# Kernel tuning notes

Measured on AMD Instinct MI355X. Metric: run time of the kernel, lower is better.

Reference implementation:

```python
import jax, jax.numpy as jnp
import numpy as np

N_NODES = 50000
F_IN = 96
HIDDEN = 128
OUT = 64
N_EDGES = 800000


def setup_inputs() -> dict:
    key = jax.random.key(0)
    ks = jax.random.split(key, 8)
    x = jax.random.normal(ks[0], (N_NODES, F_IN), dtype=jnp.float32)
    edge_index = jax.random.randint(ks[1], (2, N_EDGES), 0, N_NODES, dtype=jnp.int64)
    s = 1.0 / np.sqrt(F_IN)
    W1_rel = jax.random.uniform(ks[2], (HIDDEN, F_IN), minval=-s, maxval=s, dtype=jnp.float32)
    b1 = jax.random.uniform(ks[3], (HIDDEN,), minval=-s, maxval=s, dtype=jnp.float32)
    W1_root = jax.random.uniform(ks[4], (HIDDEN, F_IN), minval=-s, maxval=s, dtype=jnp.float32)
    s2 = 1.0 / np.sqrt(HIDDEN)
    W2_rel = jax.random.uniform(ks[5], (OUT, HIDDEN), minval=-s2, maxval=s2, dtype=jnp.float32)
    b2 = jax.random.uniform(ks[6], (OUT,), minval=-s2, maxval=s2, dtype=jnp.float32)
    W2_root = jax.random.uniform(ks[7], (OUT, HIDDEN), minval=-s2, maxval=s2, dtype=jnp.float32)
    return {"x": x, "edge_index": edge_index, "W1_rel": W1_rel, "b1": b1,
            "W1_root": W1_root, "W2_rel": W2_rel, "b2": b2, "W2_root": W2_root}


def _graph_conv(x, src, dst, mask, W_rel, b, W_root):
    # messages = x[src] (masked to remove self-loops), sum-aggregated at dst
    msgs = x[src] * mask  # [E, F]
    agg = jax.ops.segment_sum(msgs, dst, num_segments=x.shape[0])  # [N, F]
    return agg @ W_rel.T + b + x @ W_root.T


def reference(x, edge_index, W1_rel, b1, W1_root, W2_rel, b2, W2_root):
    src, dst = edge_index[0], edge_index[1]
    # remove_self_loops: zero out contributions of edges with src == dst
    mask = (src != dst).astype(x.dtype)[:, None]  # [E, 1]
    h = jax.nn.relu(_graph_conv(x, src, dst, mask, W1_rel, b1, W1_root))
    out = _graph_conv(h, src, dst, mask, W2_rel, b2, W2_root)
    return out
```

## Files before the change

kernel.cpp:

```cpp
#include <hip/hip_runtime.h>


#define N_NODES 50000
#define F_IN    96
#define HIDDEN  128
#define OUT_F   64

typedef __attribute__((ext_vector_type(8))) short short8;
typedef __attribute__((ext_vector_type(4))) float floatx4;

__device__ inline unsigned short f2bf(float f) {
    union { float f; unsigned u; } v; v.f = f;
    unsigned r = v.u + 0x7FFF + ((v.u >> 16) & 1);
    return (unsigned short)(r >> 16);
}
__device__ inline float bf2f(unsigned short b) {
    union { unsigned u; float f; } v; v.u = ((unsigned)b) << 16;
    return v.f;
}

__global__ __launch_bounds__(256) void setup_kernel(
    const float* __restrict__ x,
    const float* __restrict__ W1_rel, const float* __restrict__ W1_root,
    const float* __restrict__ W2_rel, const float* __restrict__ W2_root,
    unsigned short* __restrict__ xb, unsigned short* __restrict__ W1b,
    unsigned short* __restrict__ W2rb, unsigned short* __restrict__ W2sb,
    int* __restrict__ degz, int total8, int nzero)
{
    int i = blockIdx.x * 256 + threadIdx.x;
    if (i < total8) {
        const float4* p = (const float4*)(x + (size_t)i * 8);
        float4 v0 = p[0], v1 = p[1];
        short8 o;
        o[0] = (short)f2bf(v0.x); o[1] = (short)f2bf(v0.y);
        o[2] = (short)f2bf(v0.z); o[3] = (short)f2bf(v0.w);
        o[4] = (short)f2bf(v1.x); o[5] = (short)f2bf(v1.y);
        o[6] = (short)f2bf(v1.z); o[7] = (short)f2bf(v1.w);
        *(short8*)(xb + (size_t)i * 8) = o;
    }
    if (i < nzero) degz[i] = 0;
    if (i < 128 * 192) {
        int j = i / 192, k = i % 192;
        float v = (k < 96) ? W1_rel[j * 96 + k] : W1_root[j * 96 + k - 96];
        W1b[i] = f2bf(v);
    } else if (i < 128 * 192 + 64 * 128) {
        int i2 = i - 128 * 192;
        W2rb[i2] = f2bf(W2_rel[i2]);
    } else if (i < 128 * 192 + 2 * 64 * 128) {
        int i3 = i - 128 * 192 - 64 * 128;
        W2sb[i3] = f2bf(W2_root[i3]);
    }
}

__global__ __launch_bounds__(256) void deg_rank_kernel(
    const int* __restrict__ ei, int* __restrict__ deg,
    int* __restrict__ rank, int E)
{
    int i4 = blockIdx.x * 256 + threadIdx.x;
    int E4 = E >> 2;
    if (i4 < E4) {
        int4 s4 = ((const int4*)ei)[i4];
        int4 d4 = ((const int4*)(ei + E))[i4];
        int e0 = i4 * 4;
        int ss[4] = {s4.x, s4.y, s4.z, s4.w};
        int dd[4] = {d4.x, d4.y, d4.z, d4.w};
        #pragma unroll
        for (int k = 0; k < 4; ++k) {
            int s = ss[k], d = dd[k];
            if (s != d && (unsigned)d < (unsigned)N_NODES)
                rank[e0 + k] = atomicAdd(&deg[d], 1);
        }
    } else if (i4 == E4) {
        for (int e = E4 * 4; e < E; ++e) {
            int s = ei[e], d = ei[E + e];
            if (s != d && (unsigned)d < (unsigned)N_NODES)
                rank[e] = atomicAdd(&deg[d], 1);
        }
    }
}

__global__ __launch_bounds__(256) void alloc_kernel(
    const int* __restrict__ deg, int* __restrict__ off,
    int* __restrict__ counter, int N, int slice_size)
{
    int i = blockIdx.x * 256 + threadIdx.x;
    int lane = threadIdx.x & 63;
    int v = (i < N) ? deg[i] : 0;
    int s = v;
    #pragma unroll
    for (int d = 1; d < 64; d <<= 1) {
        int t = __shfl_up(s, d, 64);
        if (lane >= d) s += t;
    }
    int total = __shfl(s, 63, 64);
    int sl = (blockIdx.x * 256) / slice_size;
    int base = 0;
    if (lane == 63) base = atomicAdd(&counter[sl], total);
    base = __shfl(base, 63, 64);
    if (i < N) off[i] = base + s - v;
}

__global__ void scan8_kernel(const int* __restrict__ counter,
                             int* __restrict__ sbase)
{
    if (threadIdx.x == 0) {
        int run = 0;
        for (int s = 0; s < 8; ++s) { sbase[s] = run; run += counter[s]; }
    }
}

__global__ __launch_bounds__(256) void place_kernel(
    const int* __restrict__ ei, const int* __restrict__ off,
    const int* __restrict__ rank, const int* __restrict__ sbase,
    int* __restrict__ csr, int E, int slice_size)
{
    int sl = blockIdx.x & 7;
    int i4 = (blockIdx.x >> 3) * 256 + threadIdx.x;
    int sb = sbase[sl];
    int E4 = E >> 2;
    if (i4 < E4) {
        int4 d4 = ((const int4*)(ei + E))[i4];
        int e0 = i4 * 4;
        int dd[4] = {d4.x, d4.y, d4.z, d4.w};
        #pragma unroll
        for (int k = 0; k < 4; ++k) {
            int d = dd[k];
            if ((unsigned)d >= (unsigned)N_NODES) continue;
            if (d / slice_size != sl) continue;
            int e = e0 + k;
            int s = ei[e];
            if (s == d) continue;
            int p = sb + off[d] + rank[e];
            if ((unsigned)p < (unsigned)E)
                csr[p] = s;
        }
    } else if (i4 == E4) {
        for (int e = E4 * 4; e < E; ++e) {
            int d = ei[E + e];
            if ((unsigned)d >= (unsigned)N_NODES) continue;
            if (d / slice_size != sl) continue;
            int s = ei[e];
            if (s == d) continue;
            int p = sb + off[d] + rank[e];
            if ((unsigned)p < (unsigned)E)
                csr[p] = s;
        }
    }
}

template<int F>
__global__ __launch_bounds__(256) void gather_agg_bf(
    const unsigned short* __restrict__ feat, const int* __restrict__ off,
    const int* __restrict__ deg, const int* __restrict__ sbase,
    const int* __restrict__ csr, unsigned short* __restrict__ agg,
    int N, int E, int slice_size)
{
    constexpr int C = F / 8;
    int gid = blockIdx.x * 256 + threadIdx.x;
    int node = gid / C;
    int c = gid % C;
    if (node >= N) return;
    int j = sbase[node / slice_size] + off[node];
    int end = j + deg[node];
    if (j < 0) j = 0;
    if (end > E) end = E;
    float acc[8] = {};
    const unsigned short* fc = feat + c * 8;
    for (; j + 3 < end; j += 4) {
        int s0 = csr[j], s1 = csr[j + 1], s2 = csr[j + 2], s3 = csr[j + 3];
        short8 v0 = *(const short8*)(fc + (size_t)s0 * F);
        short8 v1 = *(const short8*)(fc + (size_t)s1 * F);
        short8 v2 = *(const short8*)(fc + (size_t)s2 * F);
        short8 v3 = *(const short8*)(fc + (size_t)s3 * F);
        #pragma unroll
        for (int i = 0; i < 8; ++i)
            acc[i] += (bf2f((unsigned short)v0[i]) + bf2f((unsigned short)v1[i]))
                    + (bf2f((unsigned short)v2[i]) + bf2f((unsigned short)v3[i]));
    }
    for (; j < end; ++j) {
        int s0 = csr[j];
        short8 v0 = *(const short8*)(fc + (size_t)s0 * F);
        #pragma unroll
        for (int i = 0; i < 8; ++i) acc[i] += bf2f((unsigned short)v0[i]);
    }
    short8 o;
    #pragma unroll
    for (int i = 0; i < 8; ++i) o[i] = (short)f2bf(acc[i]);
    *(short8*)(agg + (size_t)node * F + c * 8) = o;
}

template<int KT, int NO, bool SPLIT, bool RELU, bool HAS_BIAS, bool HAS_ADD, bool OUT_BF>
__global__ __launch_bounds__(256) void gemm_mfma(
    const unsigned short* __restrict__ A1, const unsigned short* __restrict__ A2,
    const unsigned short* __restrict__ W, const float* __restrict__ bias,
    const unsigned short* __restrict__ addb, void* __restrict__ out, int N)
{
    constexpr int NC = KT / 32;
    const int lane = threadIdx.x & 63;
    const int wave = threadIdx.x >> 6;
    const int node_base = blockIdx.x * 64 + wave * 16;
    const int m = lane & 15, quad = lane >> 4;
    int na = node_base + m;
    if (na >= N) na = N - 1;
    short8 a[NC];
    #pragma unroll
    for (int c = 0; c < NC; ++c) {
        if (SPLIT) {
            constexpr int HK = KT / 2;
            if (c < NC / 2)
                a[c] = *(const short8*)(A1 + (size_t)na * HK + c * 32 + quad * 8);
            else
                a[c] = *(const short8*)(A2 + (size_t)na * HK + (c - NC / 2) * 32 + quad * 8);
        } else {
            a[c] = *(const short8*)(A1 + (size_t)na * KT + c * 32 + quad * 8);
        }
    }
    #pragma unroll
    for (int jt = 0; jt < NO / 16; ++jt) {
        floatx4 acc = {0.f, 0.f, 0.f, 0.f};
        const unsigned short* wb = W + (size_t)(jt * 16 + m) * KT + quad * 8;
        #pragma unroll
        for (int c = 0; c < NC; ++c) {
            short8 b = *(const short8*)(wb + c * 32);
            acc = __builtin_amdgcn_mfma_f32_16x16x32_bf16(a[c], b, acc, 0, 0, 0);
        }
        int col = jt * 16 + m;
        float bv = HAS_BIAS ? bias[col] : 0.f;
        #pragma unroll
        for (int r = 0; r < 4; ++r) {
            int node = node_base + quad * 4 + r;
            if (node < N) {
                float v = acc[r] + bv;
                if (HAS_ADD) v += bf2f(addb[(size_t)node * NO + col]);
                if (RELU) v = fmaxf(v, 0.f);
                if (OUT_BF) ((unsigned short*)out)[(size_t)node * NO + col] = f2bf(v);
                else        ((float*)out)[(size_t)node * NO + col] = v;
            }
        }
    }
}

extern "C" void kernel_launch(void* const* d_in, const int* in_sizes, int n_in,
                              void* d_out, int out_size, void* d_ws, size_t ws_size,
                              hipStream_t stream) {
    const float* x       = (const float*)d_in[0];
    const int*   ei      = (const int*)d_in[1];
    const float* W1_rel  = (const float*)d_in[2];
    const float* b1      = (const float*)d_in[3];
    const float* W1_root = (const float*)d_in[4];
    const float* W2_rel  = (const float*)d_in[5];
    const float* b2      = (const float*)d_in[6];
    const float* W2_root = (const float*)d_in[7];
    float* out = (float*)d_out;

    const int N = in_sizes[0] / F_IN;
    const int E = in_sizes[1] / 2;
    const int slice_size = ((N + 2047) / 2048) * 256;

    char* ws = (char*)d_ws;
    size_t p = 0;
    unsigned short* xb    = (unsigned short*)(ws + p); p += (size_t)N_NODES * F_IN * 2;
    unsigned short* agg1b = (unsigned short*)(ws + p); p += (size_t)N_NODES * F_IN * 2;
    unsigned short* h     = (unsigned short*)(ws + p); p += (size_t)N_NODES * HIDDEN * 2;
    unsigned short* t     = (unsigned short*)(ws + p); p += (size_t)N_NODES * OUT_F * 2;
    unsigned short* agg2b = (unsigned short*)(ws + p); p += (size_t)N_NODES * OUT_F * 2;
    unsigned short* W1b   = (unsigned short*)(ws + p); p += (size_t)128 * 192 * 2;
    unsigned short* W2rb  = (unsigned short*)(ws + p); p += (size_t)64 * 128 * 2;
    unsigned short* W2sb  = (unsigned short*)(ws + p); p += (size_t)64 * 128 * 2;
    int* deg     = (int*)(ws + p);  p += (size_t)N_NODES * 4;
    int* counter = (int*)(ws + p);  p += 8 * 4;
    int* off     = (int*)(ws + p);  p += (size_t)N_NODES * 4;
    int* sbase   = (int*)(ws + p);  p += 8 * 4;
    int* rank    = (int*)(ws + p);  p += (size_t)800000 * 4;
    int* csr     = (int*)(ws + p);

    {
        int total8 = N * F_IN / 8;
        setup_kernel<<<(total8 + 255) / 256, 256, 0, stream>>>(
            x, W1_rel, W1_root, W2_rel, W2_root, xb, W1b, W2rb, W2sb,
            deg, total8, N + 8);
    }
    {
        int E4 = E >> 2;
        deg_rank_kernel<<<(E4 + 1 + 255) / 256, 256, 0, stream>>>(ei, deg, rank, E);
    }
    alloc_kernel<<<(N + 255) / 256, 256, 0, stream>>>(deg, off, counter, N, slice_size);
    scan8_kernel<<<1, 64, 0, stream>>>(counter, sbase);
    {
        int E4 = E >> 2;
        int bps = (E4 + 1 + 255) / 256;
        place_kernel<<<bps * 8, 256, 0, stream>>>(ei, off, rank, sbase, csr, E, slice_size);
    }

    const int gemm_blocks = (N + 63) / 64;

    {
        int total = N * (F_IN / 8);
        gather_agg_bf<F_IN><<<(total + 255) / 256, 256, 0, stream>>>(
            xb, off, deg, sbase, csr, agg1b, N, E, slice_size);
    }
    gemm_mfma<192, 128, true, true, true, false, true>
        <<<gemm_blocks, 256, 0, stream>>>(agg1b, xb, W1b, b1, nullptr, (void*)h, N);

    gemm_mfma<128, 64, false, false, false, false, true>
        <<<gemm_blocks, 256, 0, stream>>>(h, nullptr, W2rb, nullptr, nullptr, (void*)t, N);
    {
        int total = N * (OUT_F / 8);
        gather_agg_bf<OUT_F><<<(total + 255) / 256, 256, 0, stream>>>(
            t, off, deg, sbase, csr, agg2b, N, E, slice_size);
    }
    gemm_mfma<128, 64, false, false, true, true, false>
        <<<gemm_blocks, 256, 0, stream>>>(h, nullptr, W2sb, b2, agg2b, (void*)out, N);
}
```

Measured before the change: 246.2 us.

## Fuse all GNN stages into one cooperative persistent kernel with grid syncs

Replaces the nine separate kernel launches with a single cooperative persistent kernel whose phases are separated by grid.sync. It also fuses the first GEMM with the W2_rel GEMM through a shared-memory tile of h. It drops the scan8 pass by giving each slice a fixed CSR capacity region. The aim is to remove launch gaps and one full pass over h, at the cost of grid-wide barrier latency, a capped grid size, and a CSR layout that silently drops edges if one slice exceeds E/4.

Measured after the change: 687.9 us. 2.79x slower.

```diff
diff --git a/kernel.cpp b/kernel.cpp
--- a/kernel.cpp
+++ b/kernel.cpp
@@ -1,4 +1,7 @@
 #include <hip/hip_runtime.h>
+#include <hip/hip_cooperative_groups.h>
+
+namespace cg = cooperative_groups;
 
 
 #define N_NODES 50000
@@ -19,222 +22,290 @@
     return v.f;
 }
 
-__global__ __launch_bounds__(256) void setup_kernel(
-    const float* __restrict__ x,
-    const float* __restrict__ W1_rel, const float* __restrict__ W1_root,
-    const float* __restrict__ W2_rel, const float* __restrict__ W2_root,
-    unsigned short* __restrict__ xb, unsigned short* __restrict__ W1b,
-    unsigned short* __restrict__ W2rb, unsigned short* __restrict__ W2sb,
-    int* __restrict__ degz, int total8, int nzero)
-{
-    int i = blockIdx.x * 256 + threadIdx.x;
-    if (i < total8) {
-        const float4* p = (const float4*)(x + (size_t)i * 8);
-        float4 v0 = p[0], v1 = p[1];
-        short8 o;
-        o[0] = (short)f2bf(v0.x); o[1] = (short)f2bf(v0.y);
-        o[2] = (short)f2bf(v0.z); o[3] = (short)f2bf(v0.w);
-        o[4] = (short)f2bf(v1.x); o[5] = (short)f2bf(v1.y);
-        o[6] = (short)f2bf(v1.z); o[7] = (short)f2bf(v1.w);
-        *(short8*)(xb + (size_t)i * 8) = o;
-    }
-    if (i < nzero) degz[i] = 0;
-    if (i < 128 * 192) {
-        int j = i / 192, k = i % 192;
-        float v = (k < 96) ? W1_rel[j * 96 + k] : W1_root[j * 96 + k - 96];
-        W1b[i] = f2bf(v);
-    } else if (i < 128 * 192 + 64 * 128) {
-        int i2 = i - 128 * 192;
-        W2rb[i2] = f2bf(W2_rel[i2]);
-    } else if (i < 128 * 192 + 2 * 64 * 128) {
-        int i3 = i - 128 * 192 - 64 * 128;
-        W2sb[i3] = f2bf(W2_root[i3]);
-    }
-}
-
-__global__ __launch_bounds__(256) void deg_rank_kernel(
-    const int* __restrict__ ei, int* __restrict__ deg,
-    int* __restrict__ rank, int E)
-{
-    int i4 = blockIdx.x * 256 + threadIdx.x;
-    int E4 = E >> 2;
-    if (i4 < E4) {
-        int4 s4 = ((const int4*)ei)[i4];
-        int4 d4 = ((const int4*)(ei + E))[i4];
-        int e0 = i4 * 4;
-        int ss[4] = {s4.x, s4.y, s4.z, s4.w};
-        int dd[4] = {d4.x, d4.y, d4.z, d4.w};
-        #pragma unroll
-        for (int k = 0; k < 4; ++k) {
-            int s = ss[k], d = dd[k];
-            if (s != d && (unsigned)d < (unsigned)N_NODES)
-                rank[e0 + k] = atomicAdd(&deg[d], 1);
-        }
-    } else if (i4 == E4) {
-        for (int e = E4 * 4; e < E; ++e) {
-            int s = ei[e], d = ei[E + e];
-            if (s != d && (unsigned)d < (unsigned)N_NODES)
-                rank[e] = atomicAdd(&deg[d], 1);
-        }
-    }
-}
-
-__global__ __launch_bounds__(256) void alloc_kernel(
-    const int* __restrict__ deg, int* __restrict__ off,
-    int* __restrict__ counter, int N, int slice_size)
-{
-    int i = blockIdx.x * 256 + threadIdx.x;
-    int lane = threadIdx.x & 63;
-    int v = (i < N) ? deg[i] : 0;
-    int s = v;
-    #pragma unroll
-    for (int d = 1; d < 64; d <<= 1) {
-        int t = __shfl_up(s, d, 64);
-        if (lane >= d) s += t;
-    }
-    int total = __shfl(s, 63, 64);
-    int sl = (blockIdx.x * 256) / slice_size;
-    int base = 0;
-    if (lane == 63) base = atomicAdd(&counter[sl], total);
-    base = __shfl(base, 63, 64);
-    if (i < N) off[i] = base + s - v;
-}
-
-__global__ void scan8_kernel(const int* __restrict__ counter,
-                             int* __restrict__ sbase)
-{
-    if (threadIdx.x == 0) {
-        int run = 0;
-        for (int s = 0; s < 8; ++s) { sbase[s] = run; run += counter[s]; }
-    }
-}
-
-__global__ __launch_bounds__(256) void place_kernel(
-    const int* __restrict__ ei, const int* __restrict__ off,
-    const int* __restrict__ rank, const int* __restrict__ sbase,
-    int* __restrict__ csr, int E, int slice_size)
-{
-    int sl = blockIdx.x & 7;
-    int i4 = (blockIdx.x >> 3) * 256 + threadIdx.x;
-    int sb = sbase[sl];
-    int E4 = E >> 2;
-    if (i4 < E4) {
-        int4 d4 = ((const int4*)(ei + E))[i4];
-        int e0 = i4 * 4;
-        int dd[4] = {d4.x, d4.y, d4.z, d4.w};
-        #pragma unroll
-        for (int k = 0; k < 4; ++k) {
-            int d = dd[k];
-            if ((unsigned)d >= (unsigned)N_NODES) continue;
-            if (d / slice_size != sl) continue;
-            int e = e0 + k;
-            int s = ei[e];
-            if (s == d) continue;
-            int p = sb + off[d] + rank[e];
-            if ((unsigned)p < (unsigned)E)
-                csr[p] = s;
-        }
-    } else if (i4 == E4) {
-        for (int e = E4 * 4; e < E; ++e) {
-            int d = ei[E + e];
-            if ((unsigned)d >= (unsigned)N_NODES) continue;
-            if (d / slice_size != sl) continue;
-            int s = ei[e];
-            if (s == d) continue;
-            int p = sb + off[d] + rank[e];
-            if ((unsigned)p < (unsigned)E)
-                csr[p] = s;
-        }
-    }
-}
+struct MegaParams {
+    const float* x; const int* ei;
+    const float* W1_rel; const float* b1; const float* W1_root;
+    const float* W2_rel; const float* b2; const float* W2_root;
+    unsigned short* xb; unsigned short* agg1b; unsigned short* h;
+    unsigned short* t; unsigned short* agg2b;
+    unsigned short* W1b; unsigned short* W2rb; unsigned short* W2sb;
+    int* deg; int* counter; int* off; int* rank; int* csr;
+    float* out;
+    int N, E, slice_size, cap;
+};
 
 template<int F>
-__global__ __launch_bounds__(256) void gather_agg_bf(
-    const unsigned short* __restrict__ feat, const int* __restrict__ off,
-    const int* __restrict__ deg, const int* __restrict__ sbase,
-    const int* __restrict__ csr, unsigned short* __restrict__ agg,
-    int N, int E, int slice_size)
+__device__ void gather_phase(const unsigned short* __restrict__ feat,
+                             const int* __restrict__ off, const int* __restrict__ deg,
+                             const int* __restrict__ csr, unsigned short* __restrict__ agg,
+                             int N, int slice_size, int cap, int gtid, int gstride)
 {
     constexpr int C = F / 8;
-    int gid = blockIdx.x * 256 + threadIdx.x;
-    int node = gid / C;
-    int c = gid % C;
-    if (node >= N) return;
-    int j = sbase[node / slice_size] + off[node];
-    int end = j + deg[node];
-    if (j < 0) j = 0;
-    if (end > E) end = E;
-    float acc[8] = {};
-    const unsigned short* fc = feat + c * 8;
-    for (; j + 3 < end; j += 4) {
-        int s0 = csr[j], s1 = csr[j + 1], s2 = csr[j + 2], s3 = csr[j + 3];
-        short8 v0 = *(const short8*)(fc + (size_t)s0 * F);
-        short8 v1 = *(const short8*)(fc + (size_t)s1 * F);
-        short8 v2 = *(const short8*)(fc + (size_t)s2 * F);
-        short8 v3 = *(const short8*)(fc + (size_t)s3 * F);
+    const int total = N * C;
+    const int csr_total = 8 * cap;
+    for (int gid = gtid; gid < total; gid += gstride) {
+        int node = gid / C;
+        int c = gid % C;
+        int sl = node / slice_size;
+        int j = sl * cap + off[node];
+        int end = j + deg[node];
+        if (j < 0) j = 0;
+        if (end > csr_total) end = csr_total;
+        float acc[8] = {};
+        const unsigned short* fc = feat + c * 8;
+        for (; j + 3 < end; j += 4) {
+            int s0 = csr[j], s1 = csr[j + 1], s2 = csr[j + 2], s3 = csr[j + 3];
+            s0 = ((unsigned)s0 < (unsigned)N_NODES) ? s0 : 0;
+            s1 = ((unsigned)s1 < (unsigned)N_NODES) ? s1 : 0;
+            s2 = ((unsigned)s2 < (unsigned)N_NODES) ? s2 : 0;
+            s3 = ((unsigned)s3 < (unsigned)N_NODES) ? s3 : 0;
+            short8 v0 = *(const short8*)(fc + (size_t)s0 * F);
+            short8 v1 = *(const short8*)(fc + (size_t)s1 * F);
+            short8 v2 = *(const short8*)(fc + (size_t)s2 * F);
+            short8 v3 = *(const short8*)(fc + (size_t)s3 * F);
+            #pragma unroll
+            for (int i = 0; i < 8; ++i)
+                acc[i] += (bf2f((unsigned short)v0[i]) + bf2f((unsigned short)v1[i]))
+                        + (bf2f((unsigned short)v2[i]) + bf2f((unsigned short)v3[i]));
+        }
+        for (; j < end; ++j) {
+            int s0 = csr[j];
+            s0 = ((unsigned)s0 < (unsigned)N_NODES) ? s0 : 0;
+            short8 v0 = *(const short8*)(fc + (size_t)s0 * F);
+            #pragma unroll
+            for (int i = 0; i < 8; ++i) acc[i] += bf2f((unsigned short)v0[i]);
+        }
+        short8 o;
         #pragma unroll
-        for (int i = 0; i < 8; ++i)
-            acc[i] += (bf2f((unsigned short)v0[i]) + bf2f((unsigned short)v1[i]))
-                    + (bf2f((unsigned short)v2[i]) + bf2f((unsigned short)v3[i]));
-    }
-    for (; j < end; ++j) {
-        int s0 = csr[j];
-        short8 v0 = *(const short8*)(fc + (size_t)s0 * F);
-        #pragma unroll
-        for (int i = 0; i < 8; ++i) acc[i] += bf2f((unsigned short)v0[i]);
-    }
-    short8 o;
-    #pragma unroll
-    for (int i = 0; i < 8; ++i) o[i] = (short)f2bf(acc[i]);
-    *(short8*)(agg + (size_t)node * F + c * 8) = o;
-}
-
-template<int KT, int NO, bool SPLIT, bool RELU, bool HAS_BIAS, bool HAS_ADD, bool OUT_BF>
-__global__ __launch_bounds__(256) void gemm_mfma(
-    const unsigned short* __restrict__ A1, const unsigned short* __restrict__ A2,
-    const unsigned short* __restrict__ W, const float* __restrict__ bias,
-    const unsigned short* __restrict__ addb, void* __restrict__ out, int N)
+        for (int i = 0; i < 8; ++i) o[i] = (short)f2bf(acc[i]);
+        *(short8*)(agg + (size_t)node * F + c * 8) = o;
+    }
+}
+
+__global__ __launch_bounds__(256) void mega_kernel(MegaParams P)
 {
-    constexpr int NC = KT / 32;
-    const int lane = threadIdx.x & 63;
-    const int wave = threadIdx.x >> 6;
-    const int node_base = blockIdx.x * 64 + wave * 16;
+    cg::grid_group grid = cg::this_grid();
+    const int tid = threadIdx.x;
+    const int gtid = blockIdx.x * 256 + tid;
+    const int gstride = gridDim.x * 256;
+    const int lane = tid & 63;
+    const int wave = tid >> 6;
     const int m = lane & 15, quad = lane >> 4;
-    int na = node_base + m;
-    if (na >= N) na = N - 1;
-    short8 a[NC];
-    #pragma unroll
-    for (int c = 0; c < NC; ++c) {
-        if (SPLIT) {
-            constexpr int HK = KT / 2;
-            if (c < NC / 2)
-                a[c] = *(const short8*)(A1 + (size_t)na * HK + c * 32 + quad * 8);
-            else
-                a[c] = *(const short8*)(A2 + (size_t)na * HK + (c - NC / 2) * 32 + quad * 8);
-        } else {
-            a[c] = *(const short8*)(A1 + (size_t)na * KT + c * 32 + quad * 8);
-        }
-    }
-    #pragma unroll
-    for (int jt = 0; jt < NO / 16; ++jt) {
-        floatx4 acc = {0.f, 0.f, 0.f, 0.f};
-        const unsigned short* wb = W + (size_t)(jt * 16 + m) * KT + quad * 8;
-        #pragma unroll
-        for (int c = 0; c < NC; ++c) {
-            short8 b = *(const short8*)(wb + c * 32);
-            acc = __builtin_amdgcn_mfma_f32_16x16x32_bf16(a[c], b, acc, 0, 0, 0);
-        }
-        int col = jt * 16 + m;
-        float bv = HAS_BIAS ? bias[col] : 0.f;
-        #pragma unroll
-        for (int r = 0; r < 4; ++r) {
-            int node = node_base + quad * 4 + r;
-            if (node < N) {
-                float v = acc[r] + bv;
-                if (HAS_ADD) v += bf2f(addb[(size_t)node * NO + col]);
-                if (RELU) v = fmaxf(v, 0.f);
-                if (OUT_BF) ((unsigned short*)out)[(size_t)node * NO + col] = f2bf(v);
-                else        ((float*)out)[(size_t)node * NO + col] = v;
+    __shared__ __align__(16) unsigned short hs[4][16][136];
+
+    {
+        const int total8 = P.N * (F_IN / 8);
+        for (int i = gtid; i < total8; i += gstride) {
+            const float4* p = (const float4*)(P.x + (size_t)i * 8);
+            float4 v0 = p[0], v1 = p[1];
+            short8 o;
+            o[0] = (short)f2bf(v0.x); o[1] = (short)f2bf(v0.y);
+            o[2] = (short)f2bf(v0.z); o[3] = (short)f2bf(v0.w);
+            o[4] = (short)f2bf(v1.x); o[5] = (short)f2bf(v1.y);
+            o[6] = (short)f2bf(v1.z); o[7] = (short)f2bf(v1.w);
+            *(short8*)(P.xb + (size_t)i * 8) = o;
+        }
+        for (int i = gtid; i < P.N + 8; i += gstride) P.deg[i] = 0;
+        const int wtotal = 128 * 192 + 2 * 64 * 128;
+        for (int i = gtid; i < wtotal; i += gstride) {
+            if (i < 128 * 192) {
+                int j = i / 192, k = i % 192;
+                float v = (k < 96) ? P.W1_rel[j * 96 + k] : P.W1_root[j * 96 + k - 96];
+                P.W1b[i] = f2bf(v);
+            } else if (i < 128 * 192 + 64 * 128) {
+                int i2 = i - 128 * 192;
+                P.W2rb[i2] = f2bf(P.W2_rel[i2]);
+            } else {
+                int i3 = i - 128 * 192 - 64 * 128;
+                P.W2sb[i3] = f2bf(P.W2_root[i3]);
+            }
+        }
+    }
+    grid.sync();
+
+    {
+        const int E4 = P.E >> 2;
+        for (int i4 = gtid; i4 <= E4; i4 += gstride) {
+            if (i4 < E4) {
+                int4 s4 = ((const int4*)P.ei)[i4];
+                int4 d4 = ((const int4*)(P.ei + P.E))[i4];
+                int e0 = i4 * 4;
+                int ss[4] = {s4.x, s4.y, s4.z, s4.w};
+                int dd[4] = {d4.x, d4.y, d4.z, d4.w};
+                #pragma unroll
+                for (int k = 0; k < 4; ++k) {
+                    int s = ss[k], d = dd[k];
+                    if (s != d && (unsigned)d < (unsigned)N_NODES)
+                        P.rank[e0 + k] = atomicAdd(&P.deg[d], 1);
+                }
+            } else {
+                for (int e = E4 * 4; e < P.E; ++e) {
+                    int s = P.ei[e], d = P.ei[P.E + e];
+                    if (s != d && (unsigned)d < (unsigned)N_NODES)
+                        P.rank[e] = atomicAdd(&P.deg[d], 1);
+                }
+            }
+        }
+    }
+    grid.sync();
+
+    {
+        const int wgid = blockIdx.x * 4 + wave;
+        const int nw = gridDim.x * 4;
+        for (int base = wgid * 64; base < P.N; base += nw * 64) {
+            int i = base + lane;
+            int v = (i < P.N) ? P.deg[i] : 0;
+            int s = v;
+            #pragma unroll
+            for (int d = 1; d < 64; d <<= 1) {
+                int tt = __shfl_up(s, d, 64);
+                if (lane >= d) s += tt;
+            }
+            int total = __shfl(s, 63, 64);
+            int sl = base / P.slice_size;
+            int b0 = 0;
+            if (lane == 63) b0 = atomicAdd(&P.counter[sl], total);
+            b0 = __shfl(b0, 63, 64);
+            if (i < P.N) P.off[i] = b0 + s - v;
+        }
+    }
+    grid.sync();
+
+    {
+        const int E4 = P.E >> 2;
+        const int sl = blockIdx.x & 7;
+        const int bstride = (gridDim.x >> 3) * 256;
+        for (int i4 = (blockIdx.x >> 3) * 256 + tid; i4 <= E4; i4 += bstride) {
+            if (i4 < E4) {
+                int4 d4 = ((const int4*)(P.ei + P.E))[i4];
+                int e0 = i4 * 4;
+                int dd[4] = {d4.x, d4.y, d4.z, d4.w};
+                #pragma unroll
+                for (int k = 0; k < 4; ++k) {
+                    int d = dd[k];
+                    if ((unsigned)d >= (unsigned)N_NODES) continue;
+                    if (d / P.slice_size != sl) continue;
+                    int e = e0 + k;
+                    int s = P.ei[e];
+                    if (s == d) continue;
+                    int lp = P.off[d] + P.rank[e];
+                    if ((unsigned)lp < (unsigned)P.cap)
+                        P.csr[sl * P.cap + lp] = s;
+                }
+            } else {
+                for (int e = E4 * 4; e < P.E; ++e) {
+                    int d = P.ei[P.E + e];
+                    if ((unsigned)d >= (unsigned)N_NODES) continue;
+                    if (d / P.slice_size != sl) continue;
+                    int s = P.ei[e];
+                    if (s == d) continue;
+                    int lp = P.off[d] + P.rank[e];
+                    if ((unsigned)lp < (unsigned)P.cap)
+                        P.csr[sl * P.cap + lp] = s;
+                }
+            }
+        }
+    }
+    grid.sync();
+
+    gather_phase<F_IN>(P.xb, P.off, P.deg, P.csr, P.agg1b,
+                       P.N, P.slice_size, P.cap, gtid, gstride);
+    grid.sync();
+
+    {
+        const int ntiles = (P.N + 63) / 64;
+        for (int tile = blockIdx.x; tile < ntiles; tile += gridDim.x) {
+            const int node_base = tile * 64 + wave * 16;
+            int na = node_base + m;
+            if (na >= P.N) na = P.N - 1;
+            short8 a[6];
+            #pragma unroll
+            for (int c = 0; c < 6; ++c) {
+                if (c < 3)
+                    a[c] = *(const short8*)(P.agg1b + (size_t)na * 96 + c * 32 + quad * 8);
+                else
+                    a[c] = *(const short8*)(P.xb + (size_t)na * 96 + (c - 3) * 32 + quad * 8);
+            }
+            #pragma unroll
+            for (int jt = 0; jt < 8; ++jt) {
+                floatx4 acc = {0.f, 0.f, 0.f, 0.f};
+                const unsigned short* wb = P.W1b + (size_t)(jt * 16 + m) * 192 + quad * 8;
+                #pragma unroll
+                for (int c = 0; c < 6; ++c) {
+                    short8 b = *(const short8*)(wb + c * 32);
+                    acc = __builtin_amdgcn_mfma_f32_16x16x32_bf16(a[c], b, acc, 0, 0, 0);
+                }
+                int col = jt * 16 + m;
+                float bv = P.b1[col];
+                #pragma unroll
+                for (int r = 0; r < 4; ++r) {
+                    int node = node_base + quad * 4 + r;
+                    float v = fmaxf(acc[r] + bv, 0.f);
+                    unsigned short vb = f2bf(v);
+                    hs[wave][quad * 4 + r][col] = vb;
+                    if (node < P.N) P.h[(size_t)node * 128 + col] = vb;
+                }
+            }
+            __syncthreads();
+            short8 a2[4];
+            #pragma unroll
+            for (int c = 0; c < 4; ++c)
+                a2[c] = *(const short8*)&hs[wave][m][c * 32 + quad * 8];
+            #pragma unroll
+            for (int jt = 0; jt < 4; ++jt) {
+                floatx4 acc = {0.f, 0.f, 0.f, 0.f};
+                const unsigned short* wb = P.W2rb + (size_t)(jt * 16 + m) * 128 + quad * 8;
+                #pragma unroll
+                for (int c = 0; c < 4; ++c) {
+                    short8 b = *(const short8*)(wb + c * 32);
+                    acc = __builtin_amdgcn_mfma_f32_16x16x32_bf16(a2[c], b, acc, 0, 0, 0);
+                }
+                int col = jt * 16 + m;
+                #pragma unroll
+                for (int r = 0; r < 4; ++r) {
+                    int node = node_base + quad * 4 + r;
+                    if (node < P.N)
+                        P.t[(size_t)node * 64 + col] = f2bf(acc[r]);
+                }
+            }
+            __syncthreads();
+        }
+    }
+    grid.sync();
+
+    gather_phase<OUT_F>(P.t, P.off, P.deg, P.csr, P.agg2b,
+                        P.N, P.slice_size, P.cap, gtid, gstride);
+    grid.sync();
+
+    {
+        const int ntiles = (P.N + 63) / 64;
+        for (int tile = blockIdx.x; tile < ntiles; tile += gridDim.x) {
+            const int node_base = tile * 64 + wave * 16;
+            int na = node_base + m;
+            if (na >= P.N) na = P.N - 1;
+            short8 a[4];
+            #pragma unroll
+            for (int c = 0; c < 4; ++c)
+                a[c] = *(const short8*)(P.h + (size_t)na * 128 + c * 32 + quad * 8);
+            #pragma unroll
+            for (int jt = 0; jt < 4; ++jt) {
+                floatx4 acc = {0.f, 0.f, 0.f, 0.f};
+                const unsigned short* wb = P.W2sb + (size_t)(jt * 16 + m) * 128 + quad * 8;
+                #pragma unroll
+                for (int c = 0; c < 4; ++c) {
+                    short8 b = *(const short8*)(wb + c * 32);
+                    acc = __builtin_amdgcn_mfma_f32_16x16x32_bf16(a[c], b, acc, 0, 0, 0);
+                }
+                int col = jt * 16 + m;
+                float bv = P.b2[col];
+                #pragma unroll
+                for (int r = 0; r < 4; ++r) {
+                    int node = node_base + quad * 4 + r;
+                    if (node < P.N) {
+                        float v = acc[r] + bv + bf2f(P.agg2b[(size_t)node * 64 + col]);
+                        P.out[(size_t)node * 64 + col] = v;
+                    }
+                }
             }
         }
     }
@@ -243,72 +314,51 @@
 extern "C" void kernel_launch(void* const* d_in, const int* in_sizes, int n_in,
                               void* d_out, int out_size, void* d_ws, size_t ws_size,
                               hipStream_t stream) {
-    const float* x       = (const float*)d_in[0];
-    const int*   ei      = (const int*)d_in[1];
-    const float* W1_rel  = (const float*)d_in[2];
-    const float* b1      = (const float*)d_in[3];
-    const float* W1_root = (const float*)d_in[4];
-    const float* W2_rel  = (const float*)d_in[5];
-    const float* b2      = (const float*)d_in[6];
-    const float* W2_root = (const float*)d_in[7];
-    float* out = (float*)d_out;
-
     const int N = in_sizes[0] / F_IN;
     const int E = in_sizes[1] / 2;
-    const int slice_size = ((N + 2047) / 2048) * 256;
+
+    MegaParams P;
+    P.x       = (const float*)d_in[0];
+    P.ei      = (const int*)d_in[1];
+    P.W1_rel  = (const float*)d_in[2];
+    P.b1      = (const float*)d_in[3];
+    P.W1_root = (const float*)d_in[4];
+    P.W2_rel  = (const float*)d_in[5];
+    P.b2      = (const float*)d_in[6];
+    P.W2_root = (const float*)d_in[7];
+    P.out     = (float*)d_out;
+    P.N = N; P.E = E;
+    P.slice_size = ((N + 2047) / 2048) * 256;
+    P.cap = E / 4;
 
     char* ws = (char*)d_ws;
     size_t p = 0;
-    unsigned short* xb    = (unsigned short*)(ws + p); p += (size_t)N_NODES * F_IN * 2;
-    unsigned short* agg1b = (unsigned short*)(ws + p); p += (size_t)N_NODES * F_IN * 2;
-    unsigned short* h     = (unsigned short*)(ws + p); p += (size_t)N_NODES * HIDDEN * 2;
-    unsigned short* t     = (unsigned short*)(ws + p); p += (size_t)N_NODES * OUT_F * 2;
-    unsigned short* agg2b = (unsigned short*)(ws + p); p += (size_t)N_NODES * OUT_F * 2;
-    unsigned short* W1b   = (unsigned short*)(ws + p); p += (size_t)128 * 192 * 2;
-    unsigned short* W2rb  = (unsigned short*)(ws + p); p += (size_t)64 * 128 * 2;
-    unsigned short* W2sb  = (unsigned short*)(ws + p); p += (size_t)64 * 128 * 2;
-    int* deg     = (int*)(ws + p);  p += (size_t)N_NODES * 4;
-    int* counter = (int*)(ws + p);  p += 8 * 4;
-    int* off     = (int*)(ws + p);  p += (size_t)N_NODES * 4;
-    int* sbase   = (int*)(ws + p);  p += 8 * 4;
-    int* rank    = (int*)(ws + p);  p += (size_t)800000 * 4;
-    int* csr     = (int*)(ws + p);
-
-    {
-        int total8 = N * F_IN / 8;
-        setup_kernel<<<(total8 + 255) / 256, 256, 0, stream>>>(
-            x, W1_rel, W1_root, W2_rel, W2_root, xb, W1b, W2rb, W2sb,
-            deg, total8, N + 8);
-    }
-    {
-        int E4 = E >> 2;
-        deg_rank_kernel<<<(E4 + 1 + 255) / 256, 256, 0, stream>>>(ei, deg, rank, E);
-    }
-    alloc_kernel<<<(N + 255) / 256, 256, 0, stream>>>(deg, off, counter, N, slice_size);
-    scan8_kernel<<<1, 64, 0, stream>>>(counter, sbase);
-    {
-        int E4 = E >> 2;
-        int bps = (E4 + 1 + 255) / 256;
-        place_kernel<<<bps * 8, 256, 0, stream>>>(ei, off, rank, sbase, csr, E, slice_size);
-    }
-
-    const int gemm_blocks = (N + 63) / 64;
-
-    {
-        int total = N * (F_IN / 8);
-        gather_agg_bf<F_IN><<<(total + 255) / 256, 256, 0, stream>>>(
-            xb, off, deg, sbase, csr, agg1b, N, E, slice_size);
-    }
-    gemm_mfma<192, 128, true, true, true, false, true>
-        <<<gemm_blocks, 256, 0, stream>>>(agg1b, xb, W1b, b1, nullptr, (void*)h, N);
-
-    gemm_mfma<128, 64, false, false, false, false, true>
-        <<<gemm_blocks, 256, 0, stream>>>(h, nullptr, W2rb, nullptr, nullptr, (void*)t, N);
-    {
-        int total = N * (OUT_F / 8);
-        gather_agg_bf<OUT_F><<<(total + 255) / 256, 256, 0, stream>>>(
-            t, off, deg, sbase, csr, agg2b, N, E, slice_size);
-    }
-    gemm_mfma<128, 64, false, false, true, true, false>
-        <<<gemm_blocks, 256, 0, stream>>>(h, nullptr, W2sb, b2, agg2b, (void*)out, N);
-}
+    P.xb    = (unsigned short*)(ws + p); p += (size_t)N_NODES * F_IN * 2;
+    P.agg1b = (unsigned short*)(ws + p); p += (size_t)N_NODES * F_IN * 2;
+    P.h     = (unsigned short*)(ws + p); p += (size_t)N_NODES * HIDDEN * 2;
+    P.t     = (unsigned short*)(ws + p); p += (size_t)N_NODES * OUT_F * 2;
+    P.agg2b = (unsigned short*)(ws + p); p += (size_t)N_NODES * OUT_F * 2;
+    P.W1b   = (unsigned short*)(ws + p); p += (size_t)128 * 192 * 2;
+    P.W2rb  = (unsigned short*)(ws + p); p += (size_t)64 * 128 * 2;
+    P.W2sb  = (unsigned short*)(ws + p); p += (size_t)64 * 128 * 2;
+    P.deg     = (int*)(ws + p); p += (size_t)N_NODES * 4;
+    P.counter = (int*)(ws + p); p += 8 * 4;
+    P.off     = (int*)(ws + p); p += (size_t)N_NODES * 4;
+    P.rank    = (int*)(ws + p); p += (size_t)800000 * 4;
+    P.csr     = (int*)(ws + p); p += (size_t)2 * 800000 * 4;
+
+    int occ = 0;
+    hipOccupancyMaxActiveBlocksPerMultiprocessor(&occ, mega_kernel, 256, 0);
+    if (occ < 1) occ = 1;
+    int dev = 0, ncu = 0;
+    hipGetDevice(&dev);
+    hipDeviceGetAttribute(&ncu, hipDeviceAttributeMultiprocessorCount, dev);
+    if (ncu < 1) ncu = 256;
+    long long g = (long long)occ * ncu;
+    if (g > 1024) g = 1024;
+    int grid = (int)(g & ~7LL);
+    if (grid < 8) grid = 8;
+
+    void* args[] = { &P };
+    hipLaunchCooperativeKernel(mega_kernel, dim3(grid), dim3(256), args, 0, stream);
+}
```

## Fuse neighbor gathers into GEMM tiles and drop slice-base scan kernel

Applied to the files above, without the earlier changes.

The neighbor aggregation for both layers now runs inside the GEMM kernels. Each block gathers the aggregated rows for its 64 nodes into shared memory and feeds them straight to MFMA, so the agg1/agg2 global buffers and two launches go away. The CSR is laid out as fixed-capacity per-slice regions (cap = E/4), which removes the scan8 kernel and the sbase lookup. In exchange the CSR buffer is larger, and overflow is silently dropped if a slice exceeds cap. Source indices are also now clamped.

After: 242.2 us. About the same (-1.6%).

```diff
diff --git a/kernel.cpp b/kernel.cpp
--- a/kernel.cpp
+++ b/kernel.cpp
@@ -100,23 +100,13 @@
     if (i < N) off[i] = base + s - v;
 }
 
-__global__ void scan8_kernel(const int* __restrict__ counter,
-                             int* __restrict__ sbase)
-{
-    if (threadIdx.x == 0) {
-        int run = 0;
-        for (int s = 0; s < 8; ++s) { sbase[s] = run; run += counter[s]; }
-    }
-}
-
 __global__ __launch_bounds__(256) void place_kernel(
     const int* __restrict__ ei, const int* __restrict__ off,
-    const int* __restrict__ rank, const int* __restrict__ sbase,
-    int* __restrict__ csr, int E, int slice_size)
+    const int* __restrict__ rank, int* __restrict__ csr,
+    int E, int slice_size, int cap)
 {
     int sl = blockIdx.x & 7;
     int i4 = (blockIdx.x >> 3) * 256 + threadIdx.x;
-    int sb = sbase[sl];
     int E4 = E >> 2;
     if (i4 < E4) {
         int4 d4 = ((const int4*)(ei + E))[i4];
@@ -130,9 +120,9 @@
             int e = e0 + k;
             int s = ei[e];
             if (s == d) continue;
-            int p = sb + off[d] + rank[e];
-            if ((unsigned)p < (unsigned)E)
-                csr[p] = s;
+            int lp = off[d] + rank[e];
+            if ((unsigned)lp < (unsigned)cap)
+                csr[sl * cap + lp] = s;
         }
     } else if (i4 == E4) {
         for (int e = E4 * 4; e < E; ++e) {
@@ -141,33 +131,25 @@
             if (d / slice_size != sl) continue;
             int s = ei[e];
             if (s == d) continue;
-            int p = sb + off[d] + rank[e];
-            if ((unsigned)p < (unsigned)E)
-                csr[p] = s;
+            int lp = off[d] + rank[e];
+            if ((unsigned)lp < (unsigned)cap)
+                csr[sl * cap + lp] = s;
         }
     }
 }
 
 template<int F>
-__global__ __launch_bounds__(256) void gather_agg_bf(
-    const unsigned short* __restrict__ feat, const int* __restrict__ off,
-    const int* __restrict__ deg, const int* __restrict__ sbase,
-    const int* __restrict__ csr, unsigned short* __restrict__ agg,
-    int N, int E, int slice_size)
-{
-    constexpr int C = F / 8;
-    int gid = blockIdx.x * 256 + threadIdx.x;
-    int node = gid / C;
-    int c = gid % C;
-    if (node >= N) return;
-    int j = sbase[node / slice_size] + off[node];
-    int end = j + deg[node];
-    if (j < 0) j = 0;
-    if (end > E) end = E;
-    float acc[8] = {};
-    const unsigned short* fc = feat + c * 8;
+__device__ inline void gather_row8(const unsigned short* __restrict__ feat,
+                                   const int* __restrict__ csr, int j, int end,
+                                   float* acc)
+{
+    const unsigned short* fc = feat;
     for (; j + 3 < end; j += 4) {
         int s0 = csr[j], s1 = csr[j + 1], s2 = csr[j + 2], s3 = csr[j + 3];
+        s0 = ((unsigned)s0 < (unsigned)N_NODES) ? s0 : 0;
+        s1 = ((unsigned)s1 < (unsigned)N_NODES) ? s1 : 0;
+        s2 = ((unsigned)s2 < (unsigned)N_NODES) ? s2 : 0;
+        s3 = ((unsigned)s3 < (unsigned)N_NODES) ? s3 : 0;
         short8 v0 = *(const short8*)(fc + (size_t)s0 * F);
         short8 v1 = *(const short8*)(fc + (size_t)s1 * F);
         short8 v2 = *(const short8*)(fc + (size_t)s2 * F);
@@ -179,62 +161,174 @@
     }
     for (; j < end; ++j) {
         int s0 = csr[j];
+        s0 = ((unsigned)s0 < (unsigned)N_NODES) ? s0 : 0;
         short8 v0 = *(const short8*)(fc + (size_t)s0 * F);
         #pragma unroll
         for (int i = 0; i < 8; ++i) acc[i] += bf2f((unsigned short)v0[i]);
     }
-    short8 o;
-    #pragma unroll
-    for (int i = 0; i < 8; ++i) o[i] = (short)f2bf(acc[i]);
-    *(short8*)(agg + (size_t)node * F + c * 8) = o;
-}
-
-template<int KT, int NO, bool SPLIT, bool RELU, bool HAS_BIAS, bool HAS_ADD, bool OUT_BF>
-__global__ __launch_bounds__(256) void gemm_mfma(
-    const unsigned short* __restrict__ A1, const unsigned short* __restrict__ A2,
-    const unsigned short* __restrict__ W, const float* __restrict__ bias,
-    const unsigned short* __restrict__ addb, void* __restrict__ out, int N)
-{
-    constexpr int NC = KT / 32;
+}
+
+__global__ __launch_bounds__(256) void gemm1_fused(
+    const unsigned short* __restrict__ xb, const unsigned short* __restrict__ W1b,
+    const float* __restrict__ b1, const int* __restrict__ off,
+    const int* __restrict__ deg, const int* __restrict__ csr,
+    unsigned short* __restrict__ h, int N, int slice_size, int cap)
+{
+    __shared__ __align__(16) unsigned short aggs[64][104];
+    const int tid = threadIdx.x;
+    const int tile = blockIdx.x;
+    const int node0 = tile * 64;
+    const int csr_total = 8 * cap;
+
+    #pragma unroll
+    for (int it = 0; it < 3; ++it) {
+        int task = tid + it * 256;
+        int nl = task / 12, c = task % 12;
+        int node = node0 + nl;
+        float acc[8] = {};
+        if (node < N) {
+            int sl = node / slice_size;
+            int j = sl * cap + off[node];
+            int end = j + deg[node];
+            if (j < 0) j = 0;
+            if (end > csr_total) end = csr_total;
+            gather_row8<F_IN>(xb + c * 8, csr, j, end, acc);
+        }
+        short8 o;
+        #pragma unroll
+        for (int i = 0; i < 8; ++i) o[i] = (short)f2bf(acc[i]);
+        *(short8*)&aggs[nl][c * 8] = o;
+    }
+    __syncthreads();
+
+    const int lane = tid & 63;
+    const int wave = tid >> 6;
+    const int m = lane & 15, quad = lane >> 4;
+    const int node_base = node0 + wave * 16;
+    int na = node_base + m;
+    if (na >= N) na = N - 1;
+    short8 a[6];
+    #pragma unroll
+    for (int c = 0; c < 3; ++c)
+        a[c] = *(const short8*)&aggs[wave * 16 + m][c * 32 + quad * 8];
+    #pragma unroll
+    for (int c = 0; c < 3; ++c)
+        a[3 + c] = *(const short8*)(xb + (size_t)na * 96 + c * 32 + quad * 8);
+    #pragma unroll
+    for (int jt = 0; jt < 8; ++jt) {
+        floatx4 acc = {0.f, 0.f, 0.f, 0.f};
+        const unsigned short* wb = W1b + (size_t)(jt * 16 + m) * 192 + quad * 8;
+        #pragma unroll
+        for (int c = 0; c < 6; ++c) {
+            short8 b = *(const short8*)(wb + c * 32);
+            acc = __builtin_amdgcn_mfma_f32_16x16x32_bf16(a[c], b, acc, 0, 0, 0);
+        }
+        int col = jt * 16 + m;
+        float bv = b1[col];
+        #pragma unroll
+        for (int r = 0; r < 4; ++r) {
+            int node = node_base + quad * 4 + r;
+            if (node < N)
+                h[(size_t)node * 128 + col] = f2bf(fmaxf(acc[r] + bv, 0.f));
+        }
+    }
+}
+
+__global__ __launch_bounds__(256) void gemm2_kernel(
+    const unsigned short* __restrict__ h, const unsigned short* __restrict__ W2rb,
+    unsigned short* __restrict__ t, int N)
+{
     const int lane = threadIdx.x & 63;
     const int wave = threadIdx.x >> 6;
     const int node_base = blockIdx.x * 64 + wave * 16;
     const int m = lane & 15, quad = lane >> 4;
     int na = node_base + m;
     if (na >= N) na = N - 1;
-    short8 a[NC];
-    #pragma unroll
-    for (int c = 0; c < NC; ++c) {
-        if (SPLIT) {
-            constexpr int HK = KT / 2;
-            if (c < NC / 2)
-                a[c] = *(const short8*)(A1 + (size_t)na * HK + c * 32 + quad * 8);
-            else
-                a[c] = *(const short8*)(A2 + (size_t)na * HK + (c - NC / 2) * 32 + quad * 8);
-        } else {
-            a[c] = *(const short8*)(A1 + (size_t)na * KT + c * 32 + quad * 8);
-        }
-    }
-    #pragma unroll
-    for (int jt = 0; jt < NO / 16; ++jt) {
+    short8 a[4];
+    #pragma unroll
+    for (int c = 0; c < 4; ++c)
+        a[c] = *(const short8*)(h + (size_t)na * 128 + c * 32 + quad * 8);
+    #pragma unroll
+    for (int jt = 0; jt < 4; ++jt) {
         floatx4 acc = {0.f, 0.f, 0.f, 0.f};
-        const unsigned short* wb = W + (size_t)(jt * 16 + m) * KT + quad * 8;
-        #pragma unroll
-        for (int c = 0; c < NC; ++c) {
+        const unsigned short* wb = W2rb + (size_t)(jt * 16 + m) * 128 + quad * 8;
+        #pragma unroll
+        for (int c = 0; c < 4; ++c) {
             short8 b = *(const short8*)(wb + c * 32);
             acc = __builtin_amdgcn_mfma_f32_16x16x32_bf16(a[c], b, acc, 0, 0, 0);
         }
         int col = jt * 16 + m;
-        float bv = HAS_BIAS ? bias[col] : 0.f;
+        #pragma unroll
+        for (int r = 0; r < 4; ++r) {
+            int node = node_base + quad * 4 + r;
+            if (node < N)
+                t[(size_t)node * 64 + col] = f2bf(acc[r]);
+        }
+    }
+}
+
+__global__ __launch_bounds__(256) void gemm3_fused(
+    const unsigned short* __restrict__ h, const unsigned short* __restrict__ tfeat,
+    const unsigned short* __restrict__ W2sb, const float* __restrict__ b2,
+    const int* __restrict__ off, const int* __restrict__ deg,
+    const int* __restrict__ csr, float* __restrict__ out,
+    int N, int slice_size, int cap)
+{
+    __shared__ __align__(16) unsigned short agg2s[64][72];
+    const int tid = threadIdx.x;
+    const int tile = blockIdx.x;
+    const int node0 = tile * 64;
+    const int csr_total = 8 * cap;
+
+    #pragma unroll
+    for (int it = 0; it < 2; ++it) {
+        int task = tid + it * 256;
+        int nl = task / 8, c = task % 8;
+        int node = node0 + nl;
+        float acc[8] = {};
+        if (node < N) {
+            int sl = node / slice_size;
+            int j = sl * cap + off[node];
+            int end = j + deg[node];
+            if (j < 0) j = 0;
+            if (end > csr_total) end = csr_total;
+            gather_row8<OUT_F>(tfeat + c * 8, csr, j, end, acc);
+        }
+        short8 o;
+        #pragma unroll
+        for (int i = 0; i < 8; ++i) o[i] = (short)f2bf(acc[i]);
+        *(short8*)&agg2s[nl][c * 8] = o;
+    }
+    __syncthreads();
+
+    const int lane = tid & 63;
+    const int wave = tid >> 6;
+    const int m = lane & 15, quad = lane >> 4;
+    const int node_base = node0 + wave * 16;
+    int na = node_base + m;
+    if (na >= N) na = N - 1;
+    short8 a[4];
+    #pragma unroll
+    for (int c = 0; c < 4; ++c)
+        a[c] = *(const short8*)(h + (size_t)na * 128 + c * 32 + quad * 8);
+    #pragma unroll
+    for (int jt = 0; jt < 4; ++jt) {
+        floatx4 acc = {0.f, 0.f, 0.f, 0.f};
+        const unsigned short* wb = W2sb + (size_t)(jt * 16 + m) * 128 + quad * 8;
+        #pragma unroll
+        for (int c = 0; c < 4; ++c) {
+            short8 b = *(const short8*)(wb + c * 32);
+            acc = __builtin_amdgcn_mfma_f32_16x16x32_bf16(a[c], b, acc, 0, 0, 0);
+        }
+        int col = jt * 16 + m;
+        float bv = b2[col];
         #pragma unroll
         for (int r = 0; r < 4; ++r) {
             int node = node_base + quad * 4 + r;
             if (node < N) {
-                float v = acc[r] + bv;
-                if (HAS_ADD) v += bf2f(addb[(size_t)node * NO + col]);
-                if (RELU) v = fmaxf(v, 0.f);
-                if (OUT_BF) ((unsigned short*)out)[(size_t)node * NO + col] = f2bf(v);
-                else        ((float*)out)[(size_t)node * NO + col] = v;
+                int nl = wave * 16 + quad * 4 + r;
+                float v = acc[r] + bv + bf2f(agg2s[nl][col]);
+                out[(size_t)node * 64 + col] = v;
             }
         }
     }
@@ -256,23 +350,21 @@
     const int N = in_sizes[0] / F_IN;
     const int E = in_sizes[1] / 2;
     const int slice_size = ((N + 2047) / 2048) * 256;
+    const int cap = E / 4;
 
     char* ws = (char*)d_ws;
     size_t p = 0;
-    unsigned short* xb    = (unsigned short*)(ws + p); p += (size_t)N_NODES * F_IN * 2;
-    unsigned short* agg1b = (unsigned short*)(ws + p); p += (size_t)N_NODES * F_IN * 2;
-    unsigned short* h     = (unsigned short*)(ws + p); p += (size_t)N_NODES * HIDDEN * 2;
-    unsigned short* t     = (unsigned short*)(ws + p); p += (size_t)N_NODES * OUT_F * 2;
-    unsigned short* agg2b = (unsigned short*)(ws + p); p += (size_t)N_NODES * OUT_F * 2;
-    unsigned short* W1b   = (unsigned short*)(ws + p); p += (size_t)128 * 192 * 2;
-    unsigned short* W2rb  = (unsigned short*)(ws + p); p += (size_t)64 * 128 * 2;
-    unsigned short* W2sb  = (unsigned short*)(ws + p); p += (size_t)64 * 128 * 2;
+    unsigned short* xb   = (unsigned short*)(ws + p); p += (size_t)N_NODES * F_IN * 2;
+    unsigned short* h    = (unsigned short*)(ws + p); p += (size_t)N_NODES * HIDDEN * 2;
+    unsigned short* t    = (unsigned short*)(ws + p); p += (size_t)N_NODES * OUT_F * 2;
+    unsigned short* W1b  = (unsigned short*)(ws + p); p += (size_t)128 * 192 * 2;
+    unsigned short* W2rb = (unsigned short*)(ws + p); p += (size_t)64 * 128 * 2;
+    unsigned short* W2sb = (unsigned short*)(ws + p); p += (size_t)64 * 128 * 2;
     int* deg     = (int*)(ws + p);  p += (size_t)N_NODES * 4;
     int* counter = (int*)(ws + p);  p += 8 * 4;
     int* off     = (int*)(ws + p);  p += (size_t)N_NODES * 4;
-    int* sbase   = (int*)(ws + p);  p += 8 * 4;
     int* rank    = (int*)(ws + p);  p += (size_t)800000 * 4;
-    int* csr     = (int*)(ws + p);
+    int* csr     = (int*)(ws + p);  p += (size_t)2 * 800000 * 4;
 
     {
         int total8 = N * F_IN / 8;
@@ -285,30 +377,17 @@
         deg_rank_kernel<<<(E4 + 1 + 255) / 256, 256, 0, stream>>>(ei, deg, rank, E);
     }
     alloc_kernel<<<(N + 255) / 256, 256, 0, stream>>>(deg, off, counter, N, slice_size);
-    scan8_kernel<<<1, 64, 0, stream>>>(counter, sbase);
     {
         int E4 = E >> 2;
         int bps = (E4 + 1 + 255) / 256;
-        place_kernel<<<bps * 8, 256, 0, stream>>>(ei, off, rank, sbase, csr, E, slice_size);
-    }
-
-    const int gemm_blocks = (N + 63) / 64;
-
-    {
-        int total = N * (F_IN / 8);
-        gather_agg_bf<F_IN><<<(total + 255) / 256, 256, 0, stream>>>(
-            xb, off, deg, sbase, csr, agg1b, N, E, slice_size);
-    }
-    gemm_mfma<192, 128, true, true, true, false, true>
-        <<<gemm_blocks, 256, 0, stream>>>(agg1b, xb, W1b, b1, nullptr, (void*)h, N);
-
-    gemm_mfma<128, 64, false, false, false, false, true>
-        <<<gemm_blocks, 256, 0, stream>>>(h, nullptr, W2rb, nullptr, nullptr, (void*)t, N);
-    {
-        int total = N * (OUT_F / 8);
-        gather_agg_bf<OUT_F><<<(total + 255) / 256, 256, 0, stream>>>(
-            t, off, deg, sbase, csr, agg2b, N, E, slice_size);
-    }
-    gemm_mfma<128, 64, false, false, true, true, false>
-        <<<gemm_blocks, 256, 0, stream>>>(h, nullptr, W2sb, b2, agg2b, (void*)out, N);
-}
+        place_kernel<<<bps * 8, 256, 0, stream>>>(ei, off, rank, csr, E, slice_size, cap);
+    }
+
+    const int tiles = (N + 63) / 64;
+
+    gemm1_fused<<<tiles, 256, 0, stream>>>(xb, W1b, b1, off, deg, csr,
+                                           h, N, slice_size, cap);
+    gemm2_kernel<<<tiles, 256, 0, stream>>>(h, W2rb, t, N);
+    gemm3_fused<<<tiles, 256, 0, stream>>>(h, t, W2sb, b2, off, deg, csr,
+                                           out, N, slice_size, cap);
+}
```
